# Performance work log

Hardware: AMD Instinct MI355X
Metric: run time of the kernel (lower is better)

## Reference

```python
import jax, jax.numpy as jnp
import numpy as np

DIM = 128
NUM_HEADS = 8


def setup_inputs() -> dict:
    key = jax.random.key(0)
    ks = jax.random.split(key, 5)
    B, L, C = 4, 16384, DIM
    x = jax.random.normal(ks[0], (B, L, C), dtype=jnp.float32)
    # Linear params (stored as (in, out) so y = x @ W + b)
    w_qkv = jax.random.normal(ks[1], (C, 3 * C), dtype=jnp.float32) * (C ** -0.5)
    b_qkv = jax.random.normal(ks[2], (3 * C,), dtype=jnp.float32) * 0.02
    w_proj = jax.random.normal(ks[3], (C, C), dtype=jnp.float32) * (C ** -0.5)
    b_proj = jax.random.normal(ks[4], (C,), dtype=jnp.float32) * 0.02
    return {"x": x, "w_qkv": w_qkv, "b_qkv": b_qkv, "w_proj": w_proj, "b_proj": b_proj}


def reference(x, w_qkv, b_qkv, w_proj, b_proj):
    B, L, C = x.shape
    H = NUM_HEADS
    hd = C // H
    scale = C ** -0.5  # note: torch code scales by dim**-0.5, not head_dim**-0.5

    qkv = x @ w_qkv + b_qkv                      # (B, L, 3C)
    q, k, v = jnp.split(qkv, 3, axis=-1)         # each (B, L, C)

    def to_heads(t):
        return t.reshape(B, L, H, hd).transpose(0, 2, 1, 3)  # (B, H, L, hd)

    q, k, v = to_heads(q), to_heads(k), to_heads(v)

    # Per-token outer product over head_dim: (B, H, L, hd, hd)
    attn = (q * scale)[..., :, None] * k[..., None, :]
    attn = jax.nn.softmax(attn, axis=-1)

    # attn @ v per token: (B, H, L, hd)
    out = jnp.einsum("bhlij,bhlj->bhli", attn, v)
    out = out.transpose(0, 2, 1, 3).reshape(B, L, C)  # (B, L, C)
    return out @ w_proj + b_proj
```

## Files before the change

### kernel.cpp

```cpp
#include <hip/hip_runtime.h>


typedef __attribute__((ext_vector_type(8))) short bf16x8;
typedef __attribute__((ext_vector_type(4))) float f32x4;
typedef __attribute__((ext_vector_type(4))) unsigned int u32x4;

#define TILE_M 32
#define QKV_STRIDE_F 388
#define O_STRIDE 136

__device__ __forceinline__ unsigned short f2bf(float f) {
    unsigned int u = __builtin_bit_cast(unsigned int, f);
    u += 0x8000u;
    return (unsigned short)(u >> 16);
}
__device__ __forceinline__ unsigned int pkbf(float lo, float hi) {
    unsigned int a = __builtin_bit_cast(unsigned int, lo) + 0x8000u;
    unsigned int b = __builtin_bit_cast(unsigned int, hi) + 0x8000u;
    return __builtin_amdgcn_perm(b, a, 0x07060302u);
}

__global__ void prep_weights(const float* __restrict__ wqkv,
                             const float* __restrict__ wproj,
                             unsigned short* __restrict__ wqkvT,
                             unsigned short* __restrict__ wprojT) {
    int idx = blockIdx.x * 256 + threadIdx.x;
    if (idx < 384 * 128) {
        int n = idx >> 7, k = idx & 127;
        wqkvT[idx] = f2bf(wqkv[k * 384 + n]);
    }
    if (idx < 128 * 128) {
        int n = idx >> 7, k = idx & 127;
        wprojT[idx] = f2bf(wproj[k * 128 + n]);
    }
}

__global__ __launch_bounds__(256, 3) void fused_channel_attn(
    const float* __restrict__ x,
    const unsigned short* __restrict__ wqkvT,
    const float* __restrict__ bqkv,
    const unsigned short* __restrict__ wprojT,
    const float* __restrict__ bproj,
    float* __restrict__ out)
{
    __shared__ __align__(16) float us_f[TILE_M * QKV_STRIDE_F];
    unsigned short* us_o = (unsigned short*)us_f;

    const int tid  = threadIdx.x;
    const int lane = tid & 63;
    const int wave = tid >> 6;
    const int col  = lane & 15;
    const int quad = lane >> 4;
    const long base_tok = (long)blockIdx.x * TILE_M;

    const int nb = wave * 6;

    float4 xf[2][4][2];
#pragma unroll
    for (int m = 0; m < 2; ++m) {
        const float* xrow = x + (base_tok + m * 16 + col) * 128;
#pragma unroll
        for (int ks = 0; ks < 4; ++ks) {
            const float4* p = (const float4*)(xrow + ks * 32 + quad * 8);
            xf[m][ks][0] = p[0];
            xf[m][ks][1] = p[1];
        }
    }
    bf16x8 afr[2][4];
#pragma unroll
    for (int m = 0; m < 2; ++m)
#pragma unroll
        for (int ks = 0; ks < 4; ++ks) {
            float4 f0 = xf[m][ks][0], f1 = xf[m][ks][1];
            u32x4 a = {pkbf(f0.x, f0.y), pkbf(f0.z, f0.w),
                       pkbf(f1.x, f1.y), pkbf(f1.z, f1.w)};
            afr[m][ks] = __builtin_bit_cast(bf16x8, a);
        }

    f32x4 acc[2][6];
#pragma unroll
    for (int j = 0; j < 6; ++j) {
        float b = bqkv[(nb + j) * 16 + col];
        acc[0][j] = (f32x4){b, b, b, b};
        acc[1][j] = (f32x4){b, b, b, b};
    }
#pragma unroll
    for (int ks = 0; ks < 4; ++ks) {
        bf16x8 bfr[6];
#pragma unroll
        for (int j = 0; j < 6; ++j)
            bfr[j] = *(const bf16x8*)&wqkvT[((nb + j) * 16 + col) * 128 + ks * 32 + quad * 8];
#pragma unroll
        for (int j = 0; j < 6; ++j) {
            acc[0][j] = __builtin_amdgcn_mfma_f32_16x16x32_bf16(afr[0][ks], bfr[j], acc[0][j], 0, 0, 0);
            acc[1][j] = __builtin_amdgcn_mfma_f32_16x16x32_bf16(afr[1][ks], bfr[j], acc[1][j], 0, 0, 0);
        }
    }

#pragma unroll
    for (int m = 0; m < 2; ++m)
#pragma unroll
        for (int j = 0; j < 6; ++j)
#pragma unroll
            for (int r = 0; r < 4; ++r)
                us_f[(m * 16 + quad * 4 + r) * QKV_STRIDE_F + (nb + j) * 16 + col] = acc[m][j][r];
    __syncthreads();

    const int t = tid & 31;
    const int h = tid >> 5;
    const float* qkvrow = us_f + t * QKV_STRIDE_F + h * 16;

    float4 qv4[4], kv4[4], vv4[4];
#pragma unroll
    for (int c = 0; c < 4; ++c) {
        qv4[c] = ((const float4*)(qkvrow))[c];
        kv4[c] = ((const float4*)(qkvrow + 128))[c];
        vv4[c] = ((const float4*)(qkvrow + 256))[c];
    }
    __syncthreads();

    const float sl2e = 0.08838834764831845f * 1.44269504088896340f;
    float qv[16], kf[16], vf[16];
#pragma unroll
    for (int c = 0; c < 4; ++c) {
        qv[4*c] = qv4[c].x; qv[4*c+1] = qv4[c].y; qv[4*c+2] = qv4[c].z; qv[4*c+3] = qv4[c].w;
        kf[4*c] = kv4[c].x; kf[4*c+1] = kv4[c].y; kf[4*c+2] = kv4[c].z; kf[4*c+3] = kv4[c].w;
        vf[4*c] = vv4[c].x; vf[4*c+1] = vv4[c].y; vf[4*c+2] = vv4[c].z; vf[4*c+3] = vv4[c].w;
    }
    float ov[16];
#pragma unroll
    for (int i = 0; i < 16; ++i) {
        float qs = qv[i] * sl2e;
        float den = 0.f, num = 0.f;
#pragma unroll
        for (int j = 0; j < 16; ++j) {
            float e = __builtin_amdgcn_exp2f(qs * kf[j]);
            den += e;
            num = fmaf(e, vf[j], num);
        }
        ov[i] = num * __builtin_amdgcn_rcpf(den);
    }
    u32x4 o0 = {pkbf(ov[0], ov[1]), pkbf(ov[2], ov[3]), pkbf(ov[4], ov[5]), pkbf(ov[6], ov[7])};
    u32x4 o1 = {pkbf(ov[8], ov[9]), pkbf(ov[10], ov[11]), pkbf(ov[12], ov[13]), pkbf(ov[14], ov[15])};
    *(u32x4*)&us_o[t * O_STRIDE + h * 16]     = o0;
    *(u32x4*)&us_o[t * O_STRIDE + h * 16 + 8] = o1;
    __syncthreads();

    const int nb2 = wave * 2;
    bf16x8 af2[2][4];
#pragma unroll
    for (int m = 0; m < 2; ++m)
#pragma unroll
        for (int ks = 0; ks < 4; ++ks)
            af2[m][ks] = *(const bf16x8*)&us_o[(m * 16 + col) * O_STRIDE + ks * 32 + quad * 8];

    f32x4 acc2[2][2];
#pragma unroll
    for (int n = 0; n < 2; ++n) {
        float b = bproj[(nb2 + n) * 16 + col];
        acc2[0][n] = (f32x4){b, b, b, b};
        acc2[1][n] = (f32x4){b, b, b, b};
    }
#pragma unroll
    for (int ks = 0; ks < 4; ++ks) {
        bf16x8 bb[2];
#pragma unroll
        for (int n = 0; n < 2; ++n)
            bb[n] = *(const bf16x8*)&wprojT[((nb2 + n) * 16 + col) * 128 + ks * 32 + quad * 8];
#pragma unroll
        for (int n = 0; n < 2; ++n) {
            acc2[0][n] = __builtin_amdgcn_mfma_f32_16x16x32_bf16(af2[0][ks], bb[n], acc2[0][n], 0, 0, 0);
            acc2[1][n] = __builtin_amdgcn_mfma_f32_16x16x32_bf16(af2[1][ks], bb[n], acc2[1][n], 0, 0, 0);
        }
    }
#pragma unroll
    for (int m = 0; m < 2; ++m)
#pragma unroll
        for (int n = 0; n < 2; ++n)
#pragma unroll
            for (int r = 0; r < 4; ++r) {
                long tt = base_tok + m * 16 + quad * 4 + r;
                out[tt * 128 + (nb2 + n) * 16 + col] = acc2[m][n][r];
            }
}

extern "C" void kernel_launch(void* const* d_in, const int* in_sizes, int n_in,
                              void* d_out, int out_size, void* d_ws, size_t ws_size,
                              hipStream_t stream) {
    const float* x     = (const float*)d_in[0];
    const float* wqkv  = (const float*)d_in[1];
    const float* bqkv  = (const float*)d_in[2];
    const float* wproj = (const float*)d_in[3];
    const float* bproj = (const float*)d_in[4];
    float* out = (float*)d_out;

    unsigned short* wqkvT  = (unsigned short*)d_ws;
    unsigned short* wprojT = wqkvT + 384 * 128;

    prep_weights<<<192, 256, 0, stream>>>(wqkv, wproj, wqkvT, wprojT);

    const int tokens = in_sizes[0] / 128;
    fused_channel_attn<<<tokens / TILE_M, 256, 0, stream>>>(
        x, wqkvT, bqkv, wprojT, bproj, out);
}
```

Measured before the change: 132.9 us.

## Process QKV tile in two 16-row halves to halve LDS and raise occupancy

The shared QKV staging buffer is cut to 16 rows and given its own output buffer. The 32-token tile is now processed in two halves. Each half runs the softmax stage with all 256 threads, two threads per token-head splitting the query rows, and the second half's QKV write overlaps the first half's projection. Launch bounds go from 3 to 5 blocks per CU to exploit the smaller LDS footprint. The cost is extra barriers and duplicated k/v LDS reads per thread, and the register cap may cause spills.

```diff
diff --git a/kernel.cpp b/kernel.cpp
--- a/kernel.cpp
+++ b/kernel.cpp
@@ -6,6 +6,7 @@
 typedef __attribute__((ext_vector_type(4))) unsigned int u32x4;
 
 #define TILE_M 32
+#define HALF_M 16
 #define QKV_STRIDE_F 388
 #define O_STRIDE 136
 
@@ -35,7 +36,7 @@
     }
 }
 
-__global__ __launch_bounds__(256, 3) void fused_channel_attn(
+__global__ __launch_bounds__(256, 5) void fused_channel_attn(
     const float* __restrict__ x,
     const unsigned short* __restrict__ wqkvT,
     const float* __restrict__ bqkv,
@@ -43,8 +44,8 @@
     const float* __restrict__ bproj,
     float* __restrict__ out)
 {
-    __shared__ __align__(16) float us_f[TILE_M * QKV_STRIDE_F];
-    unsigned short* us_o = (unsigned short*)us_f;
+    __shared__ __align__(16) float us_f[HALF_M * QKV_STRIDE_F];
+    __shared__ __align__(16) unsigned short us_o[HALF_M * O_STRIDE];
 
     const int tid  = threadIdx.x;
     const int lane = tid & 63;
@@ -97,91 +98,98 @@
         }
     }
 
-#pragma unroll
-    for (int m = 0; m < 2; ++m)
+    const int t  = tid & 15;
+    const int h  = (tid >> 4) & 7;
+    const int ih = tid >> 7;
+    const float sl2e = 0.08838834764831845f * 1.44269504088896340f;
+
+    auto write_qkv_half = [&](int m) {
 #pragma unroll
         for (int j = 0; j < 6; ++j)
 #pragma unroll
             for (int r = 0; r < 4; ++r)
-                us_f[(m * 16 + quad * 4 + r) * QKV_STRIDE_F + (nb + j) * 16 + col] = acc[m][j][r];
-    __syncthreads();
-
-    const int t = tid & 31;
-    const int h = tid >> 5;
-    const float* qkvrow = us_f + t * QKV_STRIDE_F + h * 16;
-
-    float4 qv4[4], kv4[4], vv4[4];
-#pragma unroll
-    for (int c = 0; c < 4; ++c) {
-        qv4[c] = ((const float4*)(qkvrow))[c];
-        kv4[c] = ((const float4*)(qkvrow + 128))[c];
-        vv4[c] = ((const float4*)(qkvrow + 256))[c];
-    }
-    __syncthreads();
-
-    const float sl2e = 0.08838834764831845f * 1.44269504088896340f;
-    float qv[16], kf[16], vf[16];
-#pragma unroll
-    for (int c = 0; c < 4; ++c) {
-        qv[4*c] = qv4[c].x; qv[4*c+1] = qv4[c].y; qv[4*c+2] = qv4[c].z; qv[4*c+3] = qv4[c].w;
-        kf[4*c] = kv4[c].x; kf[4*c+1] = kv4[c].y; kf[4*c+2] = kv4[c].z; kf[4*c+3] = kv4[c].w;
-        vf[4*c] = vv4[c].x; vf[4*c+1] = vv4[c].y; vf[4*c+2] = vv4[c].z; vf[4*c+3] = vv4[c].w;
-    }
-    float ov[16];
-#pragma unroll
-    for (int i = 0; i < 16; ++i) {
-        float qs = qv[i] * sl2e;
-        float den = 0.f, num = 0.f;
-#pragma unroll
-        for (int j = 0; j < 16; ++j) {
-            float e = __builtin_amdgcn_exp2f(qs * kf[j]);
-            den += e;
-            num = fmaf(e, vf[j], num);
-        }
-        ov[i] = num * __builtin_amdgcn_rcpf(den);
-    }
-    u32x4 o0 = {pkbf(ov[0], ov[1]), pkbf(ov[2], ov[3]), pkbf(ov[4], ov[5]), pkbf(ov[6], ov[7])};
-    u32x4 o1 = {pkbf(ov[8], ov[9]), pkbf(ov[10], ov[11]), pkbf(ov[12], ov[13]), pkbf(ov[14], ov[15])};
-    *(u32x4*)&us_o[t * O_STRIDE + h * 16]     = o0;
-    *(u32x4*)&us_o[t * O_STRIDE + h * 16 + 8] = o1;
-    __syncthreads();
-
-    const int nb2 = wave * 2;
-    bf16x8 af2[2][4];
-#pragma unroll
-    for (int m = 0; m < 2; ++m)
+                us_f[(quad * 4 + r) * QKV_STRIDE_F + (nb + j) * 16 + col] = acc[m][j][r];
+    };
+
+    auto stage_b_half = [&]() {
+        const float* qkvrow = us_f + t * QKV_STRIDE_F + h * 16;
+        float4 qv4[2], kv4[4], vv4[4];
+        qv4[0] = ((const float4*)(qkvrow + ih * 8))[0];
+        qv4[1] = ((const float4*)(qkvrow + ih * 8))[1];
+#pragma unroll
+        for (int c = 0; c < 4; ++c) {
+            kv4[c] = ((const float4*)(qkvrow + 128))[c];
+            vv4[c] = ((const float4*)(qkvrow + 256))[c];
+        }
+        float qv[8], kf[16], vf[16];
+#pragma unroll
+        for (int c = 0; c < 2; ++c) {
+            qv[4*c] = qv4[c].x; qv[4*c+1] = qv4[c].y; qv[4*c+2] = qv4[c].z; qv[4*c+3] = qv4[c].w;
+        }
+#pragma unroll
+        for (int c = 0; c < 4; ++c) {
+            kf[4*c] = kv4[c].x; kf[4*c+1] = kv4[c].y; kf[4*c+2] = kv4[c].z; kf[4*c+3] = kv4[c].w;
+            vf[4*c] = vv4[c].x; vf[4*c+1] = vv4[c].y; vf[4*c+2] = vv4[c].z; vf[4*c+3] = vv4[c].w;
+        }
+        float ov[8];
+#pragma unroll
+        for (int i = 0; i < 8; ++i) {
+            float qs = qv[i] * sl2e;
+            float den = 0.f, num = 0.f;
+#pragma unroll
+            for (int j = 0; j < 16; ++j) {
+                float e = __builtin_amdgcn_exp2f(qs * kf[j]);
+                den += e;
+                num = fmaf(e, vf[j], num);
+            }
+            ov[i] = num * __builtin_amdgcn_rcpf(den);
+        }
+        u32x4 o0 = {pkbf(ov[0], ov[1]), pkbf(ov[2], ov[3]),
+                    pkbf(ov[4], ov[5]), pkbf(ov[6], ov[7])};
+        *(u32x4*)&us_o[t * O_STRIDE + h * 16 + ih * 8] = o0;
+    };
+
+    auto stage_c_half = [&](int m) {
+        const int nb2 = wave * 2;
+        bf16x8 af[4];
 #pragma unroll
         for (int ks = 0; ks < 4; ++ks)
-            af2[m][ks] = *(const bf16x8*)&us_o[(m * 16 + col) * O_STRIDE + ks * 32 + quad * 8];
-
-    f32x4 acc2[2][2];
-#pragma unroll
-    for (int n = 0; n < 2; ++n) {
-        float b = bproj[(nb2 + n) * 16 + col];
-        acc2[0][n] = (f32x4){b, b, b, b};
-        acc2[1][n] = (f32x4){b, b, b, b};
-    }
-#pragma unroll
-    for (int ks = 0; ks < 4; ++ks) {
-        bf16x8 bb[2];
-#pragma unroll
-        for (int n = 0; n < 2; ++n)
-            bb[n] = *(const bf16x8*)&wprojT[((nb2 + n) * 16 + col) * 128 + ks * 32 + quad * 8];
+            af[ks] = *(const bf16x8*)&us_o[col * O_STRIDE + ks * 32 + quad * 8];
+        f32x4 acc2[2];
 #pragma unroll
         for (int n = 0; n < 2; ++n) {
-            acc2[0][n] = __builtin_amdgcn_mfma_f32_16x16x32_bf16(af2[0][ks], bb[n], acc2[0][n], 0, 0, 0);
-            acc2[1][n] = __builtin_amdgcn_mfma_f32_16x16x32_bf16(af2[1][ks], bb[n], acc2[1][n], 0, 0, 0);
-        }
-    }
-#pragma unroll
-    for (int m = 0; m < 2; ++m)
+            float b = bproj[(nb2 + n) * 16 + col];
+            acc2[n] = (f32x4){b, b, b, b};
+        }
+#pragma unroll
+        for (int ks = 0; ks < 4; ++ks) {
+            bf16x8 bb[2];
+#pragma unroll
+            for (int n = 0; n < 2; ++n)
+                bb[n] = *(const bf16x8*)&wprojT[((nb2 + n) * 16 + col) * 128 + ks * 32 + quad * 8];
+#pragma unroll
+            for (int n = 0; n < 2; ++n)
+                acc2[n] = __builtin_amdgcn_mfma_f32_16x16x32_bf16(af[ks], bb[n], acc2[n], 0, 0, 0);
+        }
 #pragma unroll
         for (int n = 0; n < 2; ++n)
 #pragma unroll
             for (int r = 0; r < 4; ++r) {
                 long tt = base_tok + m * 16 + quad * 4 + r;
-                out[tt * 128 + (nb2 + n) * 16 + col] = acc2[m][n][r];
+                out[tt * 128 + (nb2 + n) * 16 + col] = acc2[n][r];
             }
+    };
+
+    write_qkv_half(0);
+    __syncthreads();
+    stage_b_half();
+    __syncthreads();
+    write_qkv_half(1);
+    stage_c_half(0);
+    __syncthreads();
+    stage_b_half();
+    __syncthreads();
+    stage_c_half(1);
 }
 
 extern "C" void kernel_launch(void* const* d_in, const int* in_sizes, int n_in,
```

Result: slower. 157.6 us (+18.6%).
